# Optimization experiments

Hardware: AMD Instinct MI355X
Metric: run time of the kernel (lower is better)

## Reference

```python
import jax, jax.numpy as jnp
import numpy as np

D_MODEL = 1024
NUM_HEADS = 16
D_HEAD = D_MODEL // NUM_HEADS
MAX_SEQ_LEN = 2048
THETA = 10000.0
BATCH = 2
SEQ = 2048


def _rope_tables():
    # inv_freq over even dims; emb interleaves each freq twice: [f0,f0,f1,f1,...]
    inv_freq = 1.0 / (THETA ** (jnp.arange(0, D_HEAD, 2, dtype=jnp.float32) / D_HEAD))
    t = jnp.arange(MAX_SEQ_LEN, dtype=jnp.float32)
    freqs = jnp.einsum('i,j->ij', t, inv_freq)  # [S, d_head/2]
    emb = jnp.stack((freqs, freqs), axis=-1).reshape(MAX_SEQ_LEN, D_HEAD)
    return jnp.cos(emb), jnp.sin(emb)


def _rotate_half(x):
    # pairwise interleaved rotation: (x0,x1,x2,x3,...) -> (-x1,x0,-x3,x2,...)
    xr = x.reshape(x.shape[:-1] + (D_HEAD // 2, 2))
    x1, x2 = xr[..., 0], xr[..., 1]
    return jnp.stack((-x2, x1), axis=-1).reshape(x.shape)


def setup_inputs() -> dict:
    key = jax.random.key(0)
    ks = jax.random.split(key, 5)
    std = np.sqrt(2.0 / (D_MODEL + D_MODEL)).astype(np.float32)
    return {
        'in_features': jax.random.normal(ks[0], (BATCH, SEQ, D_MODEL), dtype=jnp.float32),
        'token_positions': jnp.arange(SEQ, dtype=jnp.int64) if jax.config.jax_enable_x64 else jnp.arange(SEQ, dtype=jnp.int32),
        'wq': jax.random.normal(ks[1], (D_MODEL, D_MODEL), dtype=jnp.float32) * std,
        'wk': jax.random.normal(ks[2], (D_MODEL, D_MODEL), dtype=jnp.float32) * std,
        'wv': jax.random.normal(ks[3], (D_MODEL, D_MODEL), dtype=jnp.float32) * std,
        'wo': jax.random.normal(ks[4], (D_MODEL, D_MODEL), dtype=jnp.float32) * std,
    }


def reference(in_features, token_positions, wq, wk, wv, wo):
    b, s, _ = in_features.shape
    cos_tab, sin_tab = _rope_tables()
    cos = cos_tab[token_positions]  # [s, d_head]
    sin = sin_tab[token_positions]

    def split_heads(t):  # [b, s, d_model] -> [b, h, s, d_head]
        return t.reshape(b, s, NUM_HEADS, D_HEAD).transpose(0, 2, 1, 3)

    q = split_heads(jnp.einsum('bsd,ed->bse', in_features, wq))
    k = split_heads(jnp.einsum('bsd,ed->bse', in_features, wk))
    v = split_heads(jnp.einsum('bsd,ed->bse', in_features, wv))

    q = q * cos + _rotate_half(q) * sin
    k = k * cos + _rotate_half(k) * sin

    scale = 1.0 / np.sqrt(D_HEAD).astype(np.float32)
    scores = jnp.einsum('bhqd,bhkd->bhqk', q, k) * scale  # [b,h,s,s]
    causal = jnp.tril(jnp.ones((s, s), dtype=bool))
    scores = jnp.where(causal, scores, -jnp.inf)
    weights = jax.nn.softmax(scores, axis=-1)
    out = jnp.einsum('bhqk,bhkd->bhqd', weights, v)
    out = out.transpose(0, 2, 1, 3).reshape(b, s, D_MODEL)
    return jnp.einsum('bsd,ed->bse', out, wo)
```

## Files before the change

kernel.cpp:

```cpp
#include <hip/hip_runtime.h>


typedef __attribute__((ext_vector_type(8))) short bf16x8;
typedef __attribute__((ext_vector_type(4))) float f32x4;

__device__ __forceinline__ short f2bf(float f) {
  unsigned u = __float_as_uint(f);
  unsigned r = (u + 0x7fffu + ((u >> 16) & 1u)) >> 16;
  return (short)(r & 0xFFFFu);
}

__device__ __forceinline__ unsigned pk2(float a, float b) {
  return __builtin_amdgcn_perm(__float_as_uint(b) + 0x8000u,
                               __float_as_uint(a) + 0x8000u, 0x07060302u);
}

__device__ __forceinline__ float exp2x(float x) {
  float r;
  asm("v_exp_f32 %0, %1" : "=v"(r) : "v"(x));
  return r;
}

__device__ __forceinline__ void async16(const void* g, void* l) {
  __builtin_amdgcn_global_load_lds(
      (const __attribute__((address_space(1))) void*)g,
      (__attribute__((address_space(3))) void*)l, 16, 0, 0);
}

__device__ __forceinline__ void cstore(short* C, size_t i, float v) { C[i] = f2bf(v); }
__device__ __forceinline__ void cstore(float* C, size_t i, float v) { C[i] = v; }

__global__ void cast_all(const float4* __restrict__ X,
                         const float4* __restrict__ w0, const float4* __restrict__ w1,
                         const float4* __restrict__ w2, const float4* __restrict__ w3,
                         short* __restrict__ Xb, short* __restrict__ Wb) {
  int t = blockIdx.x * 256 + threadIdx.x;
  const float4* s;
  short4* d;
  if (t < (1 << 20)) {
    s = X + t; d = (short4*)Xb + t;
  } else {
    int u = t - (1 << 20);
    int which = u >> 18;
    s = ((which == 0) ? w0 : (which == 1) ? w1 : (which == 2) ? w2 : w3) + (u & 0x3FFFF);
    d = (short4*)Wb + u;
  }
  float4 v = *s;
  *d = make_short4(f2bf(v.x), f2bf(v.y), f2bf(v.z), f2bf(v.w));
}

enum EpiMode { EPI_ROW, EPI_KFRAG, EPI_VFRAG };

template <typename OUT, int MR, int NR, bool ROPE, EpiMode EM, bool MAPB>
__device__ __forceinline__ void gemm_core(short* __restrict__ As, short* __restrict__ Bs,
                                          const short* __restrict__ A, const short* __restrict__ B,
                                          OUT* __restrict__ C, int bm, int bn, int ldc,
                                          const int* __restrict__ pos) {
  constexpr int BM = 32 * MR, BN = 32 * NR;
  constexpr int NLD = (BM * 4 + BN * 4) / 256;
  const int tid  = threadIdx.x;
  const int lane = tid & 63, wave = tid >> 6;
  const int col  = lane & 15, quad = lane >> 4;
  const int wm = (wave & 1) * (16 * MR), wn = (wave >> 1) * (16 * NR);

  f32x4 acc[MR][NR];
#pragma unroll
  for (int i = 0; i < MR; i++)
#pragma unroll
    for (int j = 0; j < NR; j++) acc[i][j] = (f32x4){0.f, 0.f, 0.f, 0.f};

  auto stage = [&](int k0, int bu) {
#pragma unroll
    for (int c = tid; c < BM * 4; c += 256) {
      int r = c >> 2, cc = (c & 3) << 3;
      async16(A + (size_t)(bm + r) * 1024 + k0 + cc, As + bu * BM * 32 + c * 8);
    }
#pragma unroll
    for (int c = tid; c < BN * 4; c += 256) {
      int r = c >> 2, cc = (c & 3) << 3;
      int rg = bn + r;
      if (MAPB) {
        int k6 = rg & 63;
        rg = (rg & ~63) | ((k6 < 32) ? (k6 << 1) : (((k6 - 32) << 1) | 1));
      }
      async16(B + (size_t)rg * 1024 + k0 + cc, Bs + bu * BN * 32 + c * 8);
    }
  };

  stage(0, 0);
  stage(32, 1);
  if constexpr (NLD == 4) asm volatile("s_waitcnt vmcnt(4)" ::: "memory");
  else                    asm volatile("s_waitcnt vmcnt(3)" ::: "memory");
  __builtin_amdgcn_s_barrier();

  int cur = 0, nxt = 2;
  for (int it = 0; it < 32; ++it) {
    if (it < 30) stage((it + 2) * 32, nxt);
    const short* as = As + cur * (BM * 32);
    const short* bs = Bs + cur * (BN * 32);

    bf16x8 af[MR], bfr[NR];
#pragma unroll
    for (int i = 0; i < MR; i++)
      af[i] = *(const bf16x8*)(as + (wm + i * 16 + col) * 32 + quad * 8);
#pragma unroll
    for (int i = 0; i < NR; i++)
      bfr[i] = *(const bf16x8*)(bs + (wn + i * 16 + col) * 32 + quad * 8);
#pragma unroll
    for (int mi = 0; mi < MR; mi++)
#pragma unroll
      for (int ni = 0; ni < NR; ni++)
        acc[mi][ni] = __builtin_amdgcn_mfma_f32_16x16x32_bf16(af[mi], bfr[ni], acc[mi][ni], 0, 0, 0);

    if (it < 30) {
      if constexpr (NLD == 4) asm volatile("s_waitcnt vmcnt(4)" ::: "memory");
      else                    asm volatile("s_waitcnt vmcnt(3)" ::: "memory");
    } else {
      asm volatile("s_waitcnt vmcnt(0)" ::: "memory");
    }
    __builtin_amdgcn_s_barrier();
    cur = (cur == 2) ? 0 : cur + 1;
    nxt = (nxt == 2) ? 0 : nxt + 1;
  }

  if (ROPE) {
    float invf[2];
#pragma unroll
    for (int ni = 0; ni < 2; ni++) {
      int p = ni * 16 + col;
      invf[ni] = exp2f(-0.4152410118609203f * (float)p) * 0.15915494309189535f;
    }
#pragma unroll
    for (int mi = 0; mi < MR; mi++) {
#pragma unroll
      for (int r = 0; r < 4; r++) {
        int row = bm + wm + mi * 16 + quad * 4 + r;
        float fp = (float)pos[row & 2047];
#pragma unroll
        for (int ni = 0; ni < 2; ni++) {
          float rev = fp * invf[ni];
          rev -= floorf(rev);
          float sn = __builtin_amdgcn_sinf(rev);
          float cs = __builtin_amdgcn_cosf(rev);
          float x  = acc[mi][ni][r];
          float yv = acc[mi][ni + 2][r];
          acc[mi][ni][r]     = fmaf(x, cs, -yv * sn);
          acc[mi][ni + 2][r] = fmaf(yv, cs, x * sn);
        }
      }
    }
  }

  if (EM == EPI_ROW) {
#pragma unroll
    for (int mi = 0; mi < MR; mi++) {
#pragma unroll
      for (int r = 0; r < 4; r++) {
        size_t row = (size_t)(bm + wm + mi * 16 + quad * 4 + r);
#pragma unroll
        for (int ni = 0; ni < NR; ni++) {
          int cg = bn + wn + ni * 16 + col;
          cstore(C, row * ldc + cg, acc[mi][ni][r]);
        }
      }
    }
  } else if (EM == EPI_KFRAG) {
#pragma unroll
    for (int mi = 0; mi < MR; mi++) {
#pragma unroll
      for (int r = 0; r < 4; r++) {
        int m = bm + wm + mi * 16 + quad * 4 + r;
        int bq = m >> 11, key = m & 2047;
        int kt = key >> 6, nb = (key >> 4) & 3, cl = key & 15;
#pragma unroll
        for (int ni = 0; ni < NR; ni++) {
          int e = bn + wn + ni * 16 + col;
          int h = e >> 6, d = e & 63;
          size_t seg = ((((size_t)(bq * 16 + h) * 32 + kt) * 4 + nb) * 2 + (d >> 5));
          cstore((short*)C, seg * 512 + (((d >> 3) & 3) * 16 + cl) * 8 + (d & 7), acc[mi][ni][r]);
        }
      }
    }
  } else {
#pragma unroll
    for (int mi = 0; mi < MR; mi++) {
#pragma unroll
      for (int r = 0; r < 4; r++) {
        int e = bm + wm + mi * 16 + quad * 4 + r;
        int h = e >> 6, d = e & 63;
        int nb = d >> 4, cl = d & 15;
#pragma unroll
        for (int ni = 0; ni < NR; ni++) {
          int m = bn + wn + ni * 16 + col;
          int bq = m >> 11, key = m & 2047;
          int kt = key >> 6, k64 = key & 63;
          size_t seg = ((((size_t)(bq * 16 + h) * 32 + kt) * 4 + nb) * 2 + (k64 >> 5));
          cstore((short*)C, seg * 512 + (((k64 >> 3) & 3) * 16 + cl) * 8 + (k64 & 7), acc[mi][ni][r]);
        }
      }
    }
  }
}

__global__ __launch_bounds__(256, 3) void qkv_gemm(const short* __restrict__ Xb,
                                                   const short* __restrict__ Wq,
                                                   const short* __restrict__ Wk,
                                                   const short* __restrict__ Wv,
                                                   short* __restrict__ Qo,
                                                   short* __restrict__ Kf,
                                                   short* __restrict__ Vf,
                                                   const int* __restrict__ pos) {
  __shared__ __align__(16) short sm[3 * 128 * 32 + 3 * 128 * 32];
  short* As = sm;
  short* Bs = sm + 3 * 128 * 32;
  const int z = blockIdx.z;
  if (z == 0)      gemm_core<short, 4, 4, true,  EPI_ROW,   true >(As, Bs, Xb, Wq, Qo, blockIdx.x * 128, blockIdx.y * 128, 1024, pos);
  else if (z == 1) gemm_core<short, 4, 4, true,  EPI_KFRAG, true >(As, Bs, Xb, Wk, Kf, blockIdx.x * 128, blockIdx.y * 128, 0, pos);
  else             gemm_core<short, 4, 4, false, EPI_VFRAG, false>(As, Bs, Wv, Xb, Vf, blockIdx.y * 128, blockIdx.x * 128, 0, pos);
}

__global__ __launch_bounds__(256) void out_gemm(const short* __restrict__ Ctx,
                                                const short* __restrict__ Wo,
                                                float* __restrict__ C) {
  __shared__ __align__(16) short sm[3 * 64 * 32 + 3 * 128 * 32];
  gemm_core<float, 2, 4, false, EPI_ROW, false>(sm, sm + 3 * 64 * 32, Ctx, Wo, C,
                                                blockIdx.x * 64, blockIdx.y * 128, 1024, nullptr);
}

__global__ __launch_bounds__(256, 3) void flash_attn(const short* __restrict__ Q,
                                                     const short* __restrict__ Kf,
                                                     const short* __restrict__ Vf,
                                                     short* __restrict__ ctx) {
  const int y = blockIdx.y;
  const int g = y >> 3, r8 = y & 7;
  const int qt = (g == 0) ? 31 - r8 : (g == 1) ? r8 : (g == 2) ? 23 - r8 : 8 + r8;
  const int bh = blockIdx.x;
  const int b = bh >> 4, h = bh & 15;
  __shared__ __align__(16) short Ps[4][16 * 72];
  __shared__ __align__(16) short Ksm[2][4096];
  __shared__ __align__(16) short Vsm[2][4096];
  const int tid = threadIdx.x, lane = tid & 63, wave = tid >> 6;
  const int col = lane & 15, quad = lane >> 4;

  const short* Kg = Kf + (size_t)bh * 131072;
  const short* Vg = Vf + (size_t)bh * 131072;

  const float C1 = 0.18033688011112042f;
  const float mC2 = -17.31234049066756f;

  short* myPs = &Ps[wave][0];
  const int cx = col & 3;
  const int pswr0 = col * 72 + ((0 ^ cx) << 4) + quad * 4;
  const int pswr1 = col * 72 + ((1 ^ cx) << 4) + quad * 4;
  const int pswr2 = col * 72 + ((2 ^ cx) << 4) + quad * 4;
  const int pswr3 = col * 72 + ((3 ^ cx) << 4) + quad * 4;
  const int psrd0 = col * 72 + (((quad >> 1) ^ cx) << 4) + (quad & 1) * 8;
  const int psrd1 = col * 72 + ((((quad >> 1) + 2) ^ cx) << 4) + (quad & 1) * 8;

  auto stageKV = [&](int kt, short* kb, short* vb) {
    const short* kg = Kg + kt * 4096;
    const short* vg = Vg + kt * 4096;
#pragma unroll
    for (int c = tid; c < 512; c += 256) {
      async16(kg + c * 8, kb + c * 8);
      async16(vg + c * 8, vb + c * 8);
    }
  };

  const size_t qrow = (size_t)(b * 2048 + qt * 64 + wave * 16 + col);
  bf16x8 qf0 = *(const bf16x8*)(Q + qrow * 1024 + h * 64 + quad * 8);
  bf16x8 qf1 = *(const bf16x8*)(Q + qrow * 1024 + h * 64 + 32 + quad * 8);

  float l_i = 0.f;
  f32x4 o_acc[4];
#pragma unroll
  for (int i = 0; i < 4; i++) o_acc[i] = (f32x4){0.f, 0.f, 0.f, 0.f};

  short *kcur = &Ksm[0][0], *vcur = &Vsm[0][0];
  short *knxt = &Ksm[1][0], *vnxt = &Vsm[1][0];

  stageKV(0, kcur, vcur);
  asm volatile("s_waitcnt vmcnt(0)" ::: "memory");
  __builtin_amdgcn_s_barrier();

  bf16x8 afp0 = (bf16x8){0,0,0,0,0,0,0,0}, afp1 = (bf16x8){0,0,0,0,0,0,0,0};
  bf16x8 vfp[4][2];
#pragma unroll
  for (int i = 0; i < 4; i++) vfp[i][0] = vfp[i][1] = (bf16x8){0,0,0,0,0,0,0,0};

  for (int kt = 0; kt < qt; ++kt) {
    stageKV(kt + 1, knxt, vnxt);

    bf16x8 kfr[4][2];
#pragma unroll
    for (int nb = 0; nb < 4; nb++) {
      kfr[nb][0] = *(const bf16x8*)(kcur + (nb * 2 + 0) * 512 + lane * 8);
      kfr[nb][1] = *(const bf16x8*)(kcur + (nb * 2 + 1) * 512 + lane * 8);
    }

    f32x4 s_acc[4];
    __builtin_amdgcn_s_setprio(1);
#pragma unroll
    for (int nb = 0; nb < 4; nb++) {
      f32x4 z = (f32x4){0.f, 0.f, 0.f, 0.f};
      z = __builtin_amdgcn_mfma_f32_16x16x32_bf16(kfr[nb][0], qf0, z, 0, 0, 0);
      z = __builtin_amdgcn_mfma_f32_16x16x32_bf16(kfr[nb][1], qf1, z, 0, 0, 0);
      s_acc[nb] = z;
    }
    if (kt > 0) {
#pragma unroll
      for (int nb = 0; nb < 4; nb++) {
        o_acc[nb] = __builtin_amdgcn_mfma_f32_16x16x32_bf16(afp0, vfp[nb][0], o_acc[nb], 0, 0, 0);
        o_acc[nb] = __builtin_amdgcn_mfma_f32_16x16x32_bf16(afp1, vfp[nb][1], o_acc[nb], 0, 0, 0);
      }
    }
    __builtin_amdgcn_s_setprio(0);

#pragma unroll
    for (int nb = 0; nb < 4; nb++) {
      vfp[nb][0] = *(const bf16x8*)(vcur + (nb * 2 + 0) * 512 + lane * 8);
      vfp[nb][1] = *(const bf16x8*)(vcur + (nb * 2 + 1) * 512 + lane * 8);
    }

#pragma unroll
    for (int nb = 0; nb < 4; nb++) {
      float p0 = exp2x(fmaf(s_acc[nb][0], C1, mC2));
      float p1 = exp2x(fmaf(s_acc[nb][1], C1, mC2));
      float p2 = exp2x(fmaf(s_acc[nb][2], C1, mC2));
      float p3 = exp2x(fmaf(s_acc[nb][3], C1, mC2));
      int wr = (nb == 0) ? pswr0 : (nb == 1) ? pswr1 : (nb == 2) ? pswr2 : pswr3;
      *(uint2*)(myPs + wr) = make_uint2(pk2(p0, p1), pk2(p2, p3));
      l_i += (p0 + p1) + (p2 + p3);
    }
    afp0 = *(const bf16x8*)(myPs + psrd0);
    afp1 = *(const bf16x8*)(myPs + psrd1);

    asm volatile("s_waitcnt vmcnt(0)" ::: "memory");
    __builtin_amdgcn_s_barrier();
    short* t;
    t = kcur; kcur = knxt; knxt = t;
    t = vcur; vcur = vnxt; vnxt = t;
  }

  {
    const int ql = wave * 16 + col;
    const int kl = quad * 4;

    bf16x8 kfr[4][2];
#pragma unroll
    for (int nb = 0; nb < 4; nb++) {
      kfr[nb][0] = *(const bf16x8*)(kcur + (nb * 2 + 0) * 512 + lane * 8);
      kfr[nb][1] = *(const bf16x8*)(kcur + (nb * 2 + 1) * 512 + lane * 8);
    }

    f32x4 s_acc[4];
    __builtin_amdgcn_s_setprio(1);
#pragma unroll
    for (int nb = 0; nb < 4; nb++) {
      f32x4 z = (f32x4){0.f, 0.f, 0.f, 0.f};
      z = __builtin_amdgcn_mfma_f32_16x16x32_bf16(kfr[nb][0], qf0, z, 0, 0, 0);
      z = __builtin_amdgcn_mfma_f32_16x16x32_bf16(kfr[nb][1], qf1, z, 0, 0, 0);
      s_acc[nb] = z;
    }
    if (qt > 0) {
#pragma unroll
      for (int nb = 0; nb < 4; nb++) {
        o_acc[nb] = __builtin_amdgcn_mfma_f32_16x16x32_bf16(afp0, vfp[nb][0], o_acc[nb], 0, 0, 0);
        o_acc[nb] = __builtin_amdgcn_mfma_f32_16x16x32_bf16(afp1, vfp[nb][1], o_acc[nb], 0, 0, 0);
      }
    }
    __builtin_amdgcn_s_setprio(0);

#pragma unroll
    for (int nb = 0; nb < 4; nb++) {
      vfp[nb][0] = *(const bf16x8*)(vcur + (nb * 2 + 0) * 512 + lane * 8);
      vfp[nb][1] = *(const bf16x8*)(vcur + (nb * 2 + 1) * 512 + lane * 8);
    }

#pragma unroll
    for (int nb = 0; nb < 4; nb++) {
      float pv[4];
#pragma unroll
      for (int r = 0; r < 4; r++) {
        pv[r] = exp2x(fmaf(s_acc[nb][r], C1, mC2));
        if ((nb * 16 + kl + r) > ql) pv[r] = 0.f;
      }
      int wr = (nb == 0) ? pswr0 : (nb == 1) ? pswr1 : (nb == 2) ? pswr2 : pswr3;
      *(uint2*)(myPs + wr) = make_uint2(pk2(pv[0], pv[1]), pk2(pv[2], pv[3]));
      l_i += (pv[0] + pv[1]) + (pv[2] + pv[3]);
    }
    afp0 = *(const bf16x8*)(myPs + psrd0);
    afp1 = *(const bf16x8*)(myPs + psrd1);

    __builtin_amdgcn_s_setprio(1);
#pragma unroll
    for (int nb = 0; nb < 4; nb++) {
      o_acc[nb] = __builtin_amdgcn_mfma_f32_16x16x32_bf16(afp0, vfp[nb][0], o_acc[nb], 0, 0, 0);
      o_acc[nb] = __builtin_amdgcn_mfma_f32_16x16x32_bf16(afp1, vfp[nb][1], o_acc[nb], 0, 0, 0);
    }
    __builtin_amdgcn_s_setprio(0);
  }

  l_i += __shfl_xor(l_i, 16);
  l_i += __shfl_xor(l_i, 32);
  float invl = 1.0f / l_i;

#pragma unroll
  for (int r = 0; r < 4; r++) {
    float inv = __shfl(invl, quad * 4 + r);
    size_t row = (size_t)(b * 2048 + qt * 64 + wave * 16 + quad * 4 + r);
#pragma unroll
    for (int nb = 0; nb < 4; nb++)
      ctx[row * 1024 + h * 64 + nb * 16 + col] = f2bf(o_acc[nb][r] * inv);
  }
}

extern "C" void kernel_launch(void* const* d_in, const int* in_sizes, int n_in,
                              void* d_out, int out_size, void* d_ws, size_t ws_size,
                              hipStream_t stream) {
  const float* X  = (const float*)d_in[0];
  const int* pos  = (const int*)d_in[1];
  const float* wq = (const float*)d_in[2];
  const float* wk = (const float*)d_in[3];
  const float* wv = (const float*)d_in[4];
  const float* wo = (const float*)d_in[5];
  float* out = (float*)d_out;

  short* Xb  = (short*)d_ws;
  short* Wqb = Xb + (1 << 22);
  short* Wkb = Wqb + (1 << 20);
  short* Wvb = Wkb + (1 << 20);
  short* Wob = Wvb + (1 << 20);
  short* Qb  = Wob + (1 << 20);
  short* Kfb = Qb + (1 << 22);
  short* Vfb = Kfb + (1 << 22);
  short* Ctx = Vfb + (1 << 22);

  cast_all<<<8192, 256, 0, stream>>>((const float4*)X, (const float4*)wq, (const float4*)wk,
                                     (const float4*)wv, (const float4*)wo, Xb, Wqb);
  qkv_gemm<<<dim3(32, 8, 3), 256, 0, stream>>>(Xb, Wqb, Wkb, Wvb, Qb, Kfb, Vfb, pos);
  flash_attn<<<dim3(32, 32), 256, 0, stream>>>(Qb, Kfb, Vfb, Ctx);
  out_gemm<<<dim3(64, 8), 256, 0, stream>>>(Ctx, Wob, out);
}
```

Measured before the change: 166.1 us.

## Fuse Q and K projections into one GEMM sharing the X tile

Adds a gemm_qk path that computes the Q and K projections in the same block. Each X tile loaded into LDS is reused against both Wq and Wk, with RoPE and the K fragment layout applied in the epilogue. This cuts the qkv grid from 3 to 2 z-slices and removes redundant X loads. In exchange it doubles the accumulators, which raises register pressure, lowers the occupancy hint from 3 to 2, and uses more LDS.

```diff
diff --git a/kernel.cpp b/kernel.cpp
--- a/kernel.cpp
+++ b/kernel.cpp
@@ -202,7 +202,139 @@
   }
 }
 
-__global__ __launch_bounds__(256, 3) void qkv_gemm(const short* __restrict__ Xb,
+__device__ __forceinline__ void gemm_qk(short* __restrict__ As, short* __restrict__ Bqs,
+                                        short* __restrict__ Bks,
+                                        const short* __restrict__ A,
+                                        const short* __restrict__ Bq,
+                                        const short* __restrict__ Bk,
+                                        short* __restrict__ Qo, short* __restrict__ Kf,
+                                        int bm, int bn, const int* __restrict__ pos) {
+  const int tid  = threadIdx.x;
+  const int lane = tid & 63, wave = tid >> 6;
+  const int col  = lane & 15, quad = lane >> 4;
+  const int wm = (wave & 1) * 64, wn = (wave >> 1) * 64;
+
+  f32x4 aq[4][4], ak[4][4];
+#pragma unroll
+  for (int i = 0; i < 4; i++)
+#pragma unroll
+    for (int j = 0; j < 4; j++) {
+      aq[i][j] = (f32x4){0.f, 0.f, 0.f, 0.f};
+      ak[i][j] = (f32x4){0.f, 0.f, 0.f, 0.f};
+    }
+
+  auto stage = [&](int k0, int bu) {
+#pragma unroll
+    for (int c = tid; c < 512; c += 256) {
+      int r = c >> 2, cc = (c & 3) << 3;
+      async16(A + (size_t)(bm + r) * 1024 + k0 + cc, As + bu * 4096 + c * 8);
+    }
+#pragma unroll
+    for (int c = tid; c < 512; c += 256) {
+      int r = c >> 2, cc = (c & 3) << 3;
+      int rg = bn + r;
+      int k6 = rg & 63;
+      rg = (rg & ~63) | ((k6 < 32) ? (k6 << 1) : (((k6 - 32) << 1) | 1));
+      async16(Bq + (size_t)rg * 1024 + k0 + cc, Bqs + bu * 4096 + c * 8);
+      async16(Bk + (size_t)rg * 1024 + k0 + cc, Bks + bu * 4096 + c * 8);
+    }
+  };
+
+  stage(0, 0);
+  stage(32, 1);
+  asm volatile("s_waitcnt vmcnt(6)" ::: "memory");
+  __builtin_amdgcn_s_barrier();
+
+  int cur = 0, nxt = 2;
+  for (int it = 0; it < 32; ++it) {
+    if (it < 30) stage((it + 2) * 32, nxt);
+    const short* as = As + cur * 4096;
+    const short* bq = Bqs + cur * 4096;
+    const short* bk = Bks + cur * 4096;
+
+    bf16x8 af[4], bfq[4], bfk[4];
+#pragma unroll
+    for (int i = 0; i < 4; i++)
+      af[i] = *(const bf16x8*)(as + (wm + i * 16 + col) * 32 + quad * 8);
+#pragma unroll
+    for (int i = 0; i < 4; i++) {
+      bfq[i] = *(const bf16x8*)(bq + (wn + i * 16 + col) * 32 + quad * 8);
+      bfk[i] = *(const bf16x8*)(bk + (wn + i * 16 + col) * 32 + quad * 8);
+    }
+#pragma unroll
+    for (int mi = 0; mi < 4; mi++)
+#pragma unroll
+      for (int ni = 0; ni < 4; ni++) {
+        aq[mi][ni] = __builtin_amdgcn_mfma_f32_16x16x32_bf16(af[mi], bfq[ni], aq[mi][ni], 0, 0, 0);
+        ak[mi][ni] = __builtin_amdgcn_mfma_f32_16x16x32_bf16(af[mi], bfk[ni], ak[mi][ni], 0, 0, 0);
+      }
+
+    if (it < 30) asm volatile("s_waitcnt vmcnt(6)" ::: "memory");
+    else         asm volatile("s_waitcnt vmcnt(0)" ::: "memory");
+    __builtin_amdgcn_s_barrier();
+    cur = (cur == 2) ? 0 : cur + 1;
+    nxt = (nxt == 2) ? 0 : nxt + 1;
+  }
+
+  float invf[2];
+#pragma unroll
+  for (int ni = 0; ni < 2; ni++) {
+    int p = ni * 16 + col;
+    invf[ni] = exp2f(-0.4152410118609203f * (float)p) * 0.15915494309189535f;
+  }
+#pragma unroll
+  for (int mi = 0; mi < 4; mi++) {
+#pragma unroll
+    for (int r = 0; r < 4; r++) {
+      int row = bm + wm + mi * 16 + quad * 4 + r;
+      float fp = (float)pos[row & 2047];
+#pragma unroll
+      for (int ni = 0; ni < 2; ni++) {
+        float rev = fp * invf[ni];
+        rev -= floorf(rev);
+        float sn = __builtin_amdgcn_sinf(rev);
+        float cs = __builtin_amdgcn_cosf(rev);
+        float xq = aq[mi][ni][r], yq = aq[mi][ni + 2][r];
+        aq[mi][ni][r]     = fmaf(xq, cs, -yq * sn);
+        aq[mi][ni + 2][r] = fmaf(yq, cs, xq * sn);
+        float xk = ak[mi][ni][r], yk = ak[mi][ni + 2][r];
+        ak[mi][ni][r]     = fmaf(xk, cs, -yk * sn);
+        ak[mi][ni + 2][r] = fmaf(yk, cs, xk * sn);
+      }
+    }
+  }
+
+#pragma unroll
+  for (int mi = 0; mi < 4; mi++) {
+#pragma unroll
+    for (int r = 0; r < 4; r++) {
+      size_t row = (size_t)(bm + wm + mi * 16 + quad * 4 + r);
+#pragma unroll
+      for (int ni = 0; ni < 4; ni++) {
+        int cg = bn + wn + ni * 16 + col;
+        Qo[row * 1024 + cg] = f2bf(aq[mi][ni][r]);
+      }
+    }
+  }
+#pragma unroll
+  for (int mi = 0; mi < 4; mi++) {
+#pragma unroll
+    for (int r = 0; r < 4; r++) {
+      int m = bm + wm + mi * 16 + quad * 4 + r;
+      int bq2 = m >> 11, key = m & 2047;
+      int kt = key >> 6, nb = (key >> 4) & 3, cl = key & 15;
+#pragma unroll
+      for (int ni = 0; ni < 4; ni++) {
+        int e = bn + wn + ni * 16 + col;
+        int h = e >> 6, d = e & 63;
+        size_t seg = ((((size_t)(bq2 * 16 + h) * 32 + kt) * 4 + nb) * 2 + (d >> 5));
+        Kf[seg * 512 + (((d >> 3) & 3) * 16 + cl) * 8 + (d & 7)] = f2bf(ak[mi][ni][r]);
+      }
+    }
+  }
+}
+
+__global__ __launch_bounds__(256, 2) void qkv_gemm(const short* __restrict__ Xb,
                                                    const short* __restrict__ Wq,
                                                    const short* __restrict__ Wk,
                                                    const short* __restrict__ Wv,
@@ -210,13 +342,13 @@
                                                    short* __restrict__ Kf,
                                                    short* __restrict__ Vf,
                                                    const int* __restrict__ pos) {
-  __shared__ __align__(16) short sm[3 * 128 * 32 + 3 * 128 * 32];
-  short* As = sm;
-  short* Bs = sm + 3 * 128 * 32;
-  const int z = blockIdx.z;
-  if (z == 0)      gemm_core<short, 4, 4, true,  EPI_ROW,   true >(As, Bs, Xb, Wq, Qo, blockIdx.x * 128, blockIdx.y * 128, 1024, pos);
-  else if (z == 1) gemm_core<short, 4, 4, true,  EPI_KFRAG, true >(As, Bs, Xb, Wk, Kf, blockIdx.x * 128, blockIdx.y * 128, 0, pos);
-  else             gemm_core<short, 4, 4, false, EPI_VFRAG, false>(As, Bs, Wv, Xb, Vf, blockIdx.y * 128, blockIdx.x * 128, 0, pos);
+  __shared__ __align__(16) short sm[3 * 4096 * 3];
+  if (blockIdx.z == 0)
+    gemm_qk(sm, sm + 12288, sm + 24576, Xb, Wq, Wk, Qo, Kf,
+            blockIdx.x * 128, blockIdx.y * 128, pos);
+  else
+    gemm_core<short, 4, 4, false, EPI_VFRAG, false>(sm, sm + 12288, Wv, Xb, Vf,
+                                                    blockIdx.y * 128, blockIdx.x * 128, 0, pos);
 }
 
 __global__ __launch_bounds__(256) void out_gemm(const short* __restrict__ Ctx,
@@ -438,7 +570,7 @@
 
   cast_all<<<8192, 256, 0, stream>>>((const float4*)X, (const float4*)wq, (const float4*)wk,
                                      (const float4*)wv, (const float4*)wo, Xb, Wqb);
-  qkv_gemm<<<dim3(32, 8, 3), 256, 0, stream>>>(Xb, Wqb, Wkb, Wvb, Qb, Kfb, Vfb, pos);
+  qkv_gemm<<<dim3(32, 8, 2), 256, 0, stream>>>(Xb, Wqb, Wkb, Wvb, Qb, Kfb, Vfb, pos);
   flash_attn<<<dim3(32, 32), 256, 0, stream>>>(Qb, Kfb, Vfb, Ctx);
   out_gemm<<<dim3(64, 8), 256, 0, stream>>>(Ctx, Wob, out);
 }
```

Result: no change. 164.4 us (median of 3 runs) (-1.1%).
